# Performance work log

Measured on AMD Instinct MI355X. Metric: run time of the kernel, lower is better.

The kernel has to match this reference:

```python
import jax, jax.numpy as jnp
import numpy as np

UNITS = 128
INPUT_DIM = 128


def setup_inputs() -> dict:
    key = jax.random.key(0)
    k1, k2 = jax.random.split(key)
    B, T = 64, 2048
    data = jax.random.normal(k1, (B, T, INPUT_DIM), dtype=jnp.float32)
    # combined weight for [x, h] -> 4*units gates (i, f, o, g)
    W = jax.random.normal(k2, (INPUT_DIM + UNITS, 4 * UNITS), dtype=jnp.float32) * 0.05
    b = jnp.zeros((4 * UNITS,), dtype=jnp.float32)
    return {"data": data, "W": W, "b": b}


def reference(data, W, b):
    B, T, D = data.shape
    units = b.shape[0] // 4
    Wx, Wh = W[:D], W[D:]
    # Batch all input projections across time in one big GEMM (hoisted out of recurrence)
    xp = jnp.einsum('btd,dg->btg', data, Wx) + b  # [B, T, 4*units]

    def step(carry, xp_t):
        h, c = carry
        z = xp_t + h @ Wh  # [B, 4*units]
        i, f, o, g = jnp.split(z, 4, axis=-1)
        c = jax.nn.sigmoid(f) * c + jax.nn.sigmoid(i) * jnp.tanh(g)
        h = jax.nn.sigmoid(o) * jnp.tanh(c)
        return (h, c), h

    h0 = jnp.zeros((B, units), dtype=data.dtype)
    c0 = jnp.ones((B, units), dtype=data.dtype)  # original inits c to ONES
    _, hs = jax.lax.scan(step, (h0, c0), jnp.swapaxes(xp, 0, 1))  # hs: [T, B, units]
    return jnp.transpose(hs, (1, 0, 2))  # return_sequences=True -> [B, T, units]
```

## Files before the change

### kernel.cpp

```cpp
#include <hip/hip_runtime.h>
#include <cstdint>

#define UNITS 128
#define GATES 512
#define IN_DIM 128
#define BATCH 64
#define SEQ 2048
#define ROWS (BATCH * SEQ)

typedef _Float16 f16;
typedef _Float16 f16x2 __attribute__((ext_vector_type(2)));
typedef _Float16 f16x4 __attribute__((ext_vector_type(4)));
typedef _Float16 f16x8 __attribute__((ext_vector_type(8)));
typedef float    f32x4 __attribute__((ext_vector_type(4)));

static __device__ __forceinline__ float sigmoid_f(float x) {
    float e = __builtin_amdgcn_exp2f(-1.44269504f * x);
    return __builtin_amdgcn_rcpf(1.0f + e);
}
static __device__ __forceinline__ float tanh_f(float x) {
    float e = __builtin_amdgcn_exp2f(2.8853900817779268f * x);
    return 1.0f - 2.0f * __builtin_amdgcn_rcpf(1.0f + e);
}

static __device__ __forceinline__ int dot4(int a, int b, int c) {
#if __has_builtin(__builtin_amdgcn_sdot4)
    return __builtin_amdgcn_sdot4(a, b, c, false);
#else
    asm volatile("v_dot4_i32_i8 %0, %1, %2, %0" : "+v"(c) : "v"(a), "v"(b));
    return c;
#endif
}

static __device__ __forceinline__ void lds_barrier() {
    __asm__ volatile("s_waitcnt lgkmcnt(0)\n\ts_barrier" ::: "memory");
}

__global__ void wxt_kernel(const float* __restrict__ W,
                           f16* __restrict__ WxT) {
    int idx = blockIdx.x * 256 + threadIdx.x;
    int k = idx >> 9, n = idx & 511;
    WxT[n * IN_DIM + k] = (f16)W[idx];
}

__global__ __launch_bounds__(256) void xp_gemm(
        const float* __restrict__ A,
        const f16*  __restrict__ WxT,
        const float* __restrict__ bias,
        f16* __restrict__ xp) {
    const int wave = threadIdx.x >> 6;
    const int lane = threadIdx.x & 63;
    const int m16  = lane & 15;
    const int q    = lane >> 4;
    const int rowBase = blockIdx.x * 128 + wave * 32;
    const int bidx = rowBase >> 11;
    const int tBase = (rowBase & 2047) + q * 4;

    f16x8 a[2][4];
    #pragma unroll
    for (int mc = 0; mc < 2; ++mc)
        #pragma unroll
        for (int ks = 0; ks < 4; ++ks) {
            const float* p = A + (size_t)(rowBase + mc * 16 + m16) * IN_DIM
                               + ks * 32 + q * 8;
            float4 lo = *(const float4*)p;
            float4 hi = *(const float4*)(p + 4);
            f16x8 v;
            v[0] = (f16)lo.x; v[1] = (f16)lo.y; v[2] = (f16)lo.z; v[3] = (f16)lo.w;
            v[4] = (f16)hi.x; v[5] = (f16)hi.y; v[6] = (f16)hi.z; v[7] = (f16)hi.w;
            a[mc][ks] = v;
        }

    for (int nt = 0; nt < 32; ++nt) {
        f16x8 bfr[4];
        #pragma unroll
        for (int ks = 0; ks < 4; ++ks)
            bfr[ks] = *(const f16x8*)(WxT + (nt * 16 + m16) * IN_DIM + ks * 32 + q * 8);
        f32x4 acc0 = {0.f, 0.f, 0.f, 0.f}, acc1 = {0.f, 0.f, 0.f, 0.f};
        #pragma unroll
        for (int ks = 0; ks < 4; ++ks) {
            acc0 = __builtin_amdgcn_mfma_f32_16x16x32_f16(a[0][ks], bfr[ks], acc0, 0, 0, 0);
            acc1 = __builtin_amdgcn_mfma_f32_16x16x32_f16(a[1][ks], bfr[ks], acc1, 0, 0, 0);
        }
        const int col = nt * 16 + m16;
        float bv = bias[col];
        f16x4 v0, v1;
        #pragma unroll
        for (int r = 0; r < 4; ++r) {
            v0[r] = (f16)(acc0[r] + bv);
            v1[r] = (f16)(acc1[r] + bv);
        }
        f16* dst = xp + ((size_t)bidx * GATES + col) * SEQ + tBase;
        *(f16x4*)(dst)      = v0;
        *(f16x4*)(dst + 16) = v1;
    }
}

__global__ __launch_bounds__(256, 1) void lstm_scan_v7(
        const float* __restrict__ W,
        const f16* __restrict__ xpt,
        float* __restrict__ out) {
    __shared__ __align__(16) signed char hq[2][UNITS];

    const int tid  = threadIdx.x;
    const int b    = blockIdx.x;
    const int wave = tid >> 6;
    const int lane = tid & 63;
    const int half = lane >> 5;
    const int cell = wave * 32 + (lane & 31);
    const int c0   = cell + half * 256;
    const int c1   = c0 + 128;

    float mx0 = 1e-20f, mx1 = 1e-20f;
    for (int k = 0; k < 128; ++k) {
        mx0 = fmaxf(mx0, fabsf(W[(size_t)(IN_DIM + k) * GATES + c0]));
        mx1 = fmaxf(mx1, fabsf(W[(size_t)(IN_DIM + k) * GATES + c1]));
    }
    const float inv0 = 127.f / mx0, inv1 = 127.f / mx1;
    const float ms0 = mx0 * (1.f / (127.f * 127.f));
    const float ms1 = mx1 * (1.f / (127.f * 127.f));

    uint32_t wq0[32], wq1[32];
    #pragma unroll
    for (int d = 0; d < 32; ++d) {
        uint32_t p0 = 0, p1 = 0;
        #pragma unroll
        for (int j = 0; j < 4; ++j) {
            int q0 = (int)rintf(W[(size_t)(IN_DIM + 4 * d + j) * GATES + c0] * inv0);
            int q1 = (int)rintf(W[(size_t)(IN_DIM + 4 * d + j) * GATES + c1] * inv1);
            p0 |= (uint32_t)(q0 & 255) << (8 * j);
            p1 |= (uint32_t)(q1 & 255) << (8 * j);
        }
        wq0[d] = p0; wq1[d] = p1;
    }

    const float m1 = (half == 0) ? -1.44269504f : 2.8853900817779268f;
    const float A1 = (half == 0) ? 0.0f : 1.0f;
    const float B1 = (half == 0) ? 1.0f : -2.0f;

    float c = 1.0f;
    if (tid < UNITS) hq[0][tid] = 0;

    const f16* xa = xpt + ((size_t)b * GATES + c0) * SEQ;
    const f16* xb = xpt + ((size_t)b * GATES + c1) * SEQ;
    f16x8 x0cur = *(const f16x8*)(xa);
    f16x8 x1cur = *(const f16x8*)(xb);
    f16x8 x0nxt = *(const f16x8*)(xa + 8);
    f16x8 x1nxt = *(const f16x8*)(xb + 8);
    __syncthreads();

    for (int w = 0; w < SEQ / 8; ++w) {
        const int wn = (w + 2 < SEQ / 8) ? (w + 2) : (SEQ / 8 - 1);
        f16x8 x0pf = *(const f16x8*)(xa + (size_t)wn * 8);
        f16x8 x1pf = *(const f16x8*)(xb + (size_t)wn * 8);

        #pragma unroll
        for (int u = 0; u < 8; ++u) {
            const int cur = u & 1, nxt = cur ^ 1;
            const float xc0 = (float)x0cur[u];
            const float xc1 = (float)x1cur[u];

            const uint4* hsrc = (const uint4*)(&hq[cur][0]);
            uint4 hb[8];
            #pragma unroll
            for (int i = 0; i < 8; ++i) hb[i] = hsrc[i];

            int a00 = 0, a01 = 0, a10 = 0, a11 = 0;
            #pragma unroll
            for (int i = 0; i < 8; ++i) {
                const int d0 = (int)hb[i].x;
                const int d1 = (int)hb[i].y;
                const int d2 = (int)hb[i].z;
                const int d3 = (int)hb[i].w;
                const int k = 4 * i;
                if (i < 4) {
                    a00 = dot4(d0, wq0[k],     a00);
                    a10 = dot4(d0, wq1[k],     a10);
                    a00 = dot4(d1, wq0[k + 1], a00);
                    a10 = dot4(d1, wq1[k + 1], a10);
                    a00 = dot4(d2, wq0[k + 2], a00);
                    a10 = dot4(d2, wq1[k + 2], a10);
                    a00 = dot4(d3, wq0[k + 3], a00);
                    a10 = dot4(d3, wq1[k + 3], a10);
                } else {
                    a01 = dot4(d0, wq0[k],     a01);
                    a11 = dot4(d0, wq1[k],     a11);
                    a01 = dot4(d1, wq0[k + 1], a01);
                    a11 = dot4(d1, wq1[k + 1], a11);
                    a01 = dot4(d2, wq0[k + 2], a01);
                    a11 = dot4(d2, wq1[k + 2], a11);
                    a01 = dot4(d3, wq0[k + 3], a01);
                    a11 = dot4(d3, wq1[k + 3], a11);
                }
            }
            float z0 = fmaf((float)(a00 + a01), ms0, xc0);
            float z1 = fmaf((float)(a10 + a11), ms1, xc1);

            float s0 = sigmoid_f(z0);
            float e1 = __builtin_amdgcn_exp2f(m1 * z1);
            float s1 = B1 * __builtin_amdgcn_rcpf(1.0f + e1) + A1;
            float p0 = __shfl_xor(s0, 32, 64);
            float p1 = __shfl_xor(s1, 32, 64);

            float fi = (half == 0) ? s1 : p1;
            float ii = (half == 0) ? s0 : p0;
            float gg = (half == 0) ? p1 : s1;
            float oo = (half == 0) ? p0 : s0;
            c = fi * c + ii * gg;
            float h = oo * tanh_f(c);

            if (half == 0) {
                hq[nxt][cell] = (signed char)(int)rintf(h * 127.f);
            } else {
                out[((size_t)b * SEQ + w * 8 + u) * UNITS + cell] = h;
            }
            lds_barrier();
        }
        x0cur = x0nxt; x1cur = x1nxt;
        x0nxt = x0pf;  x1nxt = x1pf;
    }
}

__global__ __launch_bounds__(256, 1) void lstm_scan_fused(
        const float* __restrict__ W,
        const float* __restrict__ bias,
        const float* __restrict__ data,
        float* __restrict__ out) {
    __shared__ __align__(16) f16 h_lds[2][UNITS];
    __shared__ __align__(16) f16 x_lds[2][UNITS];

    const int tid  = threadIdx.x;
    const int b    = blockIdx.x;
    const int wave = tid >> 6;
    const int lane = tid & 63;
    const int half = lane >> 5;
    const int cell = wave * 32 + (lane & 31);
    const int c0   = cell + half * 256;
    const int c1   = c0 + 128;

    f16x2 wh0[64], wh1[64];
    #pragma unroll
    for (int k = 0; k < 64; ++k) {
        wh0[k] = f16x2{(f16)W[(size_t)(IN_DIM + 2 * k) * GATES + c0],
                       (f16)W[(size_t)(IN_DIM + 2 * k + 1) * GATES + c0]};
        wh1[k] = f16x2{(f16)W[(size_t)(IN_DIM + 2 * k) * GATES + c1],
                       (f16)W[(size_t)(IN_DIM + 2 * k + 1) * GATES + c1]};
    }
    f16x2 wxa[64], wxb[64];
    #pragma unroll
    for (int k = 0; k < 64; ++k) {
        wxa[k] = f16x2{(f16)W[(size_t)(2 * k) * GATES + c0],
                       (f16)W[(size_t)(2 * k + 1) * GATES + c0]};
        wxb[k] = f16x2{(f16)W[(size_t)(2 * k) * GATES + c1],
                       (f16)W[(size_t)(2 * k + 1) * GATES + c1]};
    }
    float bb0 = bias[c0];
    float bb1 = bias[c1];

    float c = 1.0f;
    if (tid < UNITS) h_lds[0][tid] = (f16)0.f;
    if (tid < UNITS)
        x_lds[0][tid] = (f16)data[(size_t)b * SEQ * IN_DIM + tid];
    __syncthreads();

    for (int t = 0; t < SEQ; ++t) {
        const int cur = t & 1, nxt = cur ^ 1;
        float a00 = bb0, a01 = 0.f, a10 = bb1, a11 = 0.f;

        {
            const uint4* xsrc = (const uint4*)(&x_lds[cur][0]);
            uint4 xb[16];
            #pragma unroll
            for (int i = 0; i < 16; ++i) xb[i] = xsrc[i];
            #pragma unroll
            for (int i = 0; i < 16; ++i) {
                f16x2 p0 = __builtin_bit_cast(f16x2, xb[i].x);
                f16x2 p1 = __builtin_bit_cast(f16x2, xb[i].y);
                f16x2 p2 = __builtin_bit_cast(f16x2, xb[i].z);
                f16x2 p3 = __builtin_bit_cast(f16x2, xb[i].w);
                const int k = 4 * i;
                if (i < 8) {
                    a00 = __builtin_amdgcn_fdot2(p0, wxa[k],     a00, false);
                    a10 = __builtin_amdgcn_fdot2(p0, wxb[k],     a10, false);
                    a00 = __builtin_amdgcn_fdot2(p1, wxa[k + 1], a00, false);
                    a10 = __builtin_amdgcn_fdot2(p1, wxb[k + 1], a10, false);
                    a00 = __builtin_amdgcn_fdot2(p2, wxa[k + 2], a00, false);
                    a10 = __builtin_amdgcn_fdot2(p2, wxb[k + 2], a10, false);
                    a00 = __builtin_amdgcn_fdot2(p3, wxa[k + 3], a00, false);
                    a10 = __builtin_amdgcn_fdot2(p3, wxb[k + 3], a10, false);
                } else {
                    a01 = __builtin_amdgcn_fdot2(p0, wxa[k],     a01, false);
                    a11 = __builtin_amdgcn_fdot2(p0, wxb[k],     a11, false);
                    a01 = __builtin_amdgcn_fdot2(p1, wxa[k + 1], a01, false);
                    a11 = __builtin_amdgcn_fdot2(p1, wxb[k + 1], a11, false);
                    a01 = __builtin_amdgcn_fdot2(p2, wxa[k + 2], a01, false);
                    a11 = __builtin_amdgcn_fdot2(p2, wxb[k + 2], a11, false);
                    a01 = __builtin_amdgcn_fdot2(p3, wxa[k + 3], a01, false);
                    a11 = __builtin_amdgcn_fdot2(p3, wxb[k + 3], a11, false);
                }
            }
        }
        {
            const uint4* hsrc = (const uint4*)(&h_lds[cur][0]);
            uint4 hb[16];
            #pragma unroll
            for (int i = 0; i < 16; ++i) hb[i] = hsrc[i];
            #pragma unroll
            for (int i = 0; i < 16; ++i) {
                f16x2 p0 = __builtin_bit_cast(f16x2, hb[i].x);
                f16x2 p1 = __builtin_bit_cast(f16x2, hb[i].y);
                f16x2 p2 = __builtin_bit_cast(f16x2, hb[i].z);
                f16x2 p3 = __builtin_bit_cast(f16x2, hb[i].w);
                const int k = 4 * i;
                if (i < 8) {
                    a00 = __builtin_amdgcn_fdot2(p0, wh0[k],     a00, false);
                    a10 = __builtin_amdgcn_fdot2(p0, wh1[k],     a10, false);
                    a00 = __builtin_amdgcn_fdot2(p1, wh0[k + 1], a00, false);
                    a10 = __builtin_amdgcn_fdot2(p1, wh1[k + 1], a10, false);
                    a00 = __builtin_amdgcn_fdot2(p2, wh0[k + 2], a00, false);
                    a10 = __builtin_amdgcn_fdot2(p2, wh1[k + 2], a10, false);
                    a00 = __builtin_amdgcn_fdot2(p3, wh0[k + 3], a00, false);
                    a10 = __builtin_amdgcn_fdot2(p3, wh1[k + 3], a10, false);
                } else {
                    a01 = __builtin_amdgcn_fdot2(p0, wh0[k],     a01, false);
                    a11 = __builtin_amdgcn_fdot2(p0, wh1[k],     a11, false);
                    a01 = __builtin_amdgcn_fdot2(p1, wh0[k + 1], a01, false);
                    a11 = __builtin_amdgcn_fdot2(p1, wh1[k + 1], a11, false);
                    a01 = __builtin_amdgcn_fdot2(p2, wh0[k + 2], a01, false);
                    a11 = __builtin_amdgcn_fdot2(p2, wh1[k + 2], a11, false);
                    a01 = __builtin_amdgcn_fdot2(p3, wh0[k + 3], a01, false);
                    a11 = __builtin_amdgcn_fdot2(p3, wh1[k + 3], a11, false);
                }
            }
        }
        float z0 = a00 + a01, z1 = a10 + a11;

        float s0 = sigmoid_f(z0);
        float s1 = (half == 0) ? sigmoid_f(z1) : tanh_f(z1);
        float p0 = __shfl_xor(s0, 32, 64);
        float p1 = __shfl_xor(s1, 32, 64);

        if (half == 0) {
            c = s1 * c + s0 * p1;
            float h = p0 * tanh_f(c);
            h_lds[nxt][cell] = (f16)h;
            out[((size_t)b * SEQ + t) * UNITS + cell] = h;
        }
        if (tid < UNITS) {
            int t1 = (t + 1 < SEQ) ? (t + 1) : t;
            x_lds[nxt][tid] = (f16)data[(size_t)b * SEQ * IN_DIM
                                        + (size_t)t1 * IN_DIM + tid];
        }
        lds_barrier();
    }
}

extern "C" void kernel_launch(void* const* d_in, const int* in_sizes, int n_in,
                              void* d_out, int out_size, void* d_ws, size_t ws_size,
                              hipStream_t stream) {
    const float* data = (const float*)d_in[0];
    const float* W    = (const float*)d_in[1];
    const float* bias = (const float*)d_in[2];
    float* out = (float*)d_out;

    const size_t wxt_bytes = (size_t)GATES * IN_DIM * sizeof(f16);
    const size_t xp_bytes  = (size_t)ROWS * GATES * sizeof(f16);
    if (ws_size >= wxt_bytes + xp_bytes) {
        f16* WxT = (f16*)d_ws;
        f16* xp  = (f16*)((char*)d_ws + wxt_bytes);
        hipLaunchKernelGGL(wxt_kernel, dim3(256), dim3(256), 0, stream, W, WxT);
        hipLaunchKernelGGL(xp_gemm, dim3(ROWS / 128), dim3(256), 0, stream,
                           data, WxT, bias, xp);
        hipLaunchKernelGGL(lstm_scan_v7, dim3(BATCH), dim3(256), 0, stream,
                           W, xp, out);
    } else {
        hipLaunchKernelGGL(lstm_scan_fused, dim3(BATCH), dim3(256), 0, stream,
                           W, bias, data, out);
    }
}
```

Baseline: 985.8 us.

## Map one thread per LSTM cell with all four gates, removing cross-lane shuffles

```diff
diff --git a/kernel.cpp b/kernel.cpp
--- a/kernel.cpp
+++ b/kernel.cpp
@@ -96,76 +96,80 @@
     }
 }
 
-__global__ __launch_bounds__(256, 1) void lstm_scan_v7(
+__global__ __launch_bounds__(128, 1) void lstm_scan_v8(
         const float* __restrict__ W,
         const f16* __restrict__ xpt,
         float* __restrict__ out) {
     __shared__ __align__(16) signed char hq[2][UNITS];
 
-    const int tid  = threadIdx.x;
-    const int b    = blockIdx.x;
-    const int wave = tid >> 6;
-    const int lane = tid & 63;
-    const int half = lane >> 5;
-    const int cell = wave * 32 + (lane & 31);
-    const int c0   = cell + half * 256;
-    const int c1   = c0 + 128;
-
-    float mx0 = 1e-20f, mx1 = 1e-20f;
-    for (int k = 0; k < 128; ++k) {
-        mx0 = fmaxf(mx0, fabsf(W[(size_t)(IN_DIM + k) * GATES + c0]));
-        mx1 = fmaxf(mx1, fabsf(W[(size_t)(IN_DIM + k) * GATES + c1]));
-    }
-    const float inv0 = 127.f / mx0, inv1 = 127.f / mx1;
-    const float ms0 = mx0 * (1.f / (127.f * 127.f));
-    const float ms1 = mx1 * (1.f / (127.f * 127.f));
-
-    uint32_t wq0[32], wq1[32];
-    #pragma unroll
-    for (int d = 0; d < 32; ++d) {
-        uint32_t p0 = 0, p1 = 0;
-        #pragma unroll
-        for (int j = 0; j < 4; ++j) {
-            int q0 = (int)rintf(W[(size_t)(IN_DIM + 4 * d + j) * GATES + c0] * inv0);
-            int q1 = (int)rintf(W[(size_t)(IN_DIM + 4 * d + j) * GATES + c1] * inv1);
-            p0 |= (uint32_t)(q0 & 255) << (8 * j);
-            p1 |= (uint32_t)(q1 & 255) << (8 * j);
-        }
-        wq0[d] = p0; wq1[d] = p1;
-    }
-
-    const float m1 = (half == 0) ? -1.44269504f : 2.8853900817779268f;
-    const float A1 = (half == 0) ? 0.0f : 1.0f;
-    const float B1 = (half == 0) ? 1.0f : -2.0f;
-
-    float c = 1.0f;
-    if (tid < UNITS) hq[0][tid] = 0;
-
-    const f16* xa = xpt + ((size_t)b * GATES + c0) * SEQ;
-    const f16* xb = xpt + ((size_t)b * GATES + c1) * SEQ;
-    f16x8 x0cur = *(const f16x8*)(xa);
-    f16x8 x1cur = *(const f16x8*)(xb);
-    f16x8 x0nxt = *(const f16x8*)(xa + 8);
-    f16x8 x1nxt = *(const f16x8*)(xb + 8);
+    const int j = threadIdx.x;
+    const int b = blockIdx.x;
+
+    float msI, msF, msO, msG;
+    uint32_t wqI[32], wqF[32], wqO[32], wqG[32];
+#define QCOL(ARR, MS, COL)                                                    \
+    {                                                                         \
+        const int col_ = (COL);                                               \
+        float mx_ = 1e-20f;                                                   \
+        for (int k_ = 0; k_ < 128; ++k_)                                      \
+            mx_ = fmaxf(mx_, fabsf(W[(size_t)(IN_DIM + k_) * GATES + col_]));  \
+        const float inv_ = 127.f / mx_;                                       \
+        MS = mx_ * (1.f / (127.f * 127.f));                                   \
+        _Pragma("unroll")                                                     \
+        for (int d_ = 0; d_ < 32; ++d_) {                                     \
+            uint32_t p_ = 0;                                                  \
+            _Pragma("unroll")                                                 \
+            for (int t_ = 0; t_ < 4; ++t_) {                                  \
+                int q_ = (int)rintf(                                          \
+                    W[(size_t)(IN_DIM + 4 * d_ + t_) * GATES + col_] * inv_); \
+                p_ |= (uint32_t)(q_ & 255) << (8 * t_);                       \
+            }                                                                 \
+            ARR[d_] = p_;                                                     \
+        }                                                                     \
+    }
+    QCOL(wqI, msI, j)
+    QCOL(wqF, msF, j + 128)
+    QCOL(wqO, msO, j + 256)
+    QCOL(wqG, msG, j + 384)
+#undef QCOL
+
+    float cc = 1.0f;
+    hq[0][j] = 0;
+
+    const f16* xI = xpt + ((size_t)b * GATES + j      ) * SEQ;
+    const f16* xF = xpt + ((size_t)b * GATES + j + 128) * SEQ;
+    const f16* xO = xpt + ((size_t)b * GATES + j + 256) * SEQ;
+    const f16* xG = xpt + ((size_t)b * GATES + j + 384) * SEQ;
+    f16x8 xcI = *(const f16x8*)xI,       xcF = *(const f16x8*)xF;
+    f16x8 xcO = *(const f16x8*)xO,       xcG = *(const f16x8*)xG;
+    f16x8 xnI = *(const f16x8*)(xI + 8), xnF = *(const f16x8*)(xF + 8);
+    f16x8 xnO = *(const f16x8*)(xO + 8), xnG = *(const f16x8*)(xG + 8);
     __syncthreads();
 
+    float hout[8];
     for (int w = 0; w < SEQ / 8; ++w) {
         const int wn = (w + 2 < SEQ / 8) ? (w + 2) : (SEQ / 8 - 1);
-        f16x8 x0pf = *(const f16x8*)(xa + (size_t)wn * 8);
-        f16x8 x1pf = *(const f16x8*)(xb + (size_t)wn * 8);
+        f16x8 xpI = *(const f16x8*)(xI + (size_t)wn * 8);
+        f16x8 xpF = *(const f16x8*)(xF + (size_t)wn * 8);
+        f16x8 xpO = *(const f16x8*)(xO + (size_t)wn * 8);
+        f16x8 xpG = *(const f16x8*)(xG + (size_t)wn * 8);
+
+        if (w > 0) {
+            float* ob = out + ((size_t)b * SEQ + (size_t)(w - 1) * 8) * UNITS + j;
+            #pragma unroll
+            for (int u = 0; u < 8; ++u) ob[u * UNITS] = hout[u];
+        }
 
         #pragma unroll
         for (int u = 0; u < 8; ++u) {
             const int cur = u & 1, nxt = cur ^ 1;
-            const float xc0 = (float)x0cur[u];
-            const float xc1 = (float)x1cur[u];
 
             const uint4* hsrc = (const uint4*)(&hq[cur][0]);
             uint4 hb[8];
             #pragma unroll
             for (int i = 0; i < 8; ++i) hb[i] = hsrc[i];
 
-            int a00 = 0, a01 = 0, a10 = 0, a11 = 0;
+            int aI = 0, aF = 0, aO = 0, aG = 0;
             #pragma unroll
             for (int i = 0; i < 8; ++i) {
                 const int d0 = (int)hb[i].x;
@@ -173,51 +177,49 @@
                 const int d2 = (int)hb[i].z;
                 const int d3 = (int)hb[i].w;
                 const int k = 4 * i;
-                if (i < 4) {
-                    a00 = dot4(d0, wq0[k],     a00);
-                    a10 = dot4(d0, wq1[k],     a10);
-                    a00 = dot4(d1, wq0[k + 1], a00);
-                    a10 = dot4(d1, wq1[k + 1], a10);
-                    a00 = dot4(d2, wq0[k + 2], a00);
-                    a10 = dot4(d2, wq1[k + 2], a10);
-                    a00 = dot4(d3, wq0[k + 3], a00);
-                    a10 = dot4(d3, wq1[k + 3], a10);
-                } else {
-                    a01 = dot4(d0, wq0[k],     a01);
-                    a11 = dot4(d0, wq1[k],     a11);
-                    a01 = dot4(d1, wq0[k + 1], a01);
-                    a11 = dot4(d1, wq1[k + 1], a11);
-                    a01 = dot4(d2, wq0[k + 2], a01);
-                    a11 = dot4(d2, wq1[k + 2], a11);
-                    a01 = dot4(d3, wq0[k + 3], a01);
-                    a11 = dot4(d3, wq1[k + 3], a11);
-                }
+                aI = dot4(d0, wqI[k],     aI);
+                aF = dot4(d0, wqF[k],     aF);
+                aO = dot4(d0, wqO[k],     aO);
+                aG = dot4(d0, wqG[k],     aG);
+                aI = dot4(d1, wqI[k + 1], aI);
+                aF = dot4(d1, wqF[k + 1], aF);
+                aO = dot4(d1, wqO[k + 1], aO);
+                aG = dot4(d1, wqG[k + 1], aG);
+                aI = dot4(d2, wqI[k + 2], aI);
+                aF = dot4(d2, wqF[k + 2], aF);
+                aO = dot4(d2, wqO[k + 2], aO);
+                aG = dot4(d2, wqG[k + 2], aG);
+                aI = dot4(d3, wqI[k + 3], aI);
+                aF = dot4(d3, wqF[k + 3], aF);
+                aO = dot4(d3, wqO[k + 3], aO);
+                aG = dot4(d3, wqG[k + 3], aG);
             }
-            float z0 = fmaf((float)(a00 + a01), ms0, xc0);
-            float z1 = fmaf((float)(a10 + a11), ms1, xc1);
-
-            float s0 = sigmoid_f(z0);
-            float e1 = __builtin_amdgcn_exp2f(m1 * z1);
-            float s1 = B1 * __builtin_amdgcn_rcpf(1.0f + e1) + A1;
-            float p0 = __shfl_xor(s0, 32, 64);
-            float p1 = __shfl_xor(s1, 32, 64);
-
-            float fi = (half == 0) ? s1 : p1;
-            float ii = (half == 0) ? s0 : p0;
-            float gg = (half == 0) ? p1 : s1;
-            float oo = (half == 0) ? p0 : s0;
-            c = fi * c + ii * gg;
-            float h = oo * tanh_f(c);
-
-            if (half == 0) {
-                hq[nxt][cell] = (signed char)(int)rintf(h * 127.f);
-            } else {
-                out[((size_t)b * SEQ + w * 8 + u) * UNITS + cell] = h;
-            }
+            float zI = fmaf((float)aI, msI, (float)xcI[u]);
+            float zF = fmaf((float)aF, msF, (float)xcF[u]);
+            float zO = fmaf((float)aO, msO, (float)xcO[u]);
+            float zG = fmaf((float)aG, msG, (float)xcG[u]);
+
+            float si = sigmoid_f(zI);
+            float sf = sigmoid_f(zF);
+            float so = sigmoid_f(zO);
+            float eg = __builtin_amdgcn_exp2f(2.8853900817779268f * zG);
+            float tg = 1.f - 2.f * __builtin_amdgcn_rcpf(1.f + eg);
+
+            cc = sf * cc + si * tg;
+            float ec = __builtin_amdgcn_exp2f(2.8853900817779268f * cc);
+            float rc = __builtin_amdgcn_rcpf(1.f + ec);
+            float h127 = fmaf(-254.f * so, rc, 127.f * so);
+            hq[nxt][j] = (signed char)(int)rintf(h127);
+            hout[u] = h127 * 7.874015748031496e-3f;
             lds_barrier();
         }
-        x0cur = x0nxt; x1cur = x1nxt;
-        x0nxt = x0pf;  x1nxt = x1pf;
+        xcI = xnI; xcF = xnF; xcO = xnO; xcG = xnG;
+        xnI = xpI; xnF = xpF; xnO = xpO; xnG = xpG;
+    }
+    {
+        float* ob = out + ((size_t)b * SEQ + (size_t)(SEQ / 8 - 1) * 8) * UNITS + j;
+        #pragma unroll
+        for (int u = 0; u < 8; ++u) ob[u * UNITS] = hout[u];
     }
 }
 
@@ -371,7 +373,7 @@
         hipLaunchKernelGGL(wxt_kernel, dim3(256), dim3(256), 0, stream, W, WxT);
         hipLaunchKernelGGL(xp_gemm, dim3(ROWS / 128), dim3(256), 0, stream,
                            data, WxT, bias, xp);
-        hipLaunchKernelGGL(lstm_scan_v7, dim3(BATCH), dim3(256), 0, stream,
+        hipLaunchKernelGGL(lstm_scan_v8, dim3(BATCH), dim3(128), 0, stream,
                            W, xp, out);
     } else {
         hipLaunchKernelGGL(lstm_scan_fused, dim3(BATCH), dim3(256), 0, stream,
```

Measured after the change: 1.208 ms. +22.6%, slower.
